# Kernel tuning notes

Measured on AMD Instinct MI355X. Metric: run time of the kernel, lower is better.

## Reference

```python
import jax, jax.numpy as jnp
import numpy as np
import math

N, E, F, H = 8000, 64000, 64, 10
C = F  # out_channels == in_channels in Drug's RAGCN
INV_SQRT_F = 1.0 / math.sqrt(F)


def _glorot(key, shape):
    lim = math.sqrt(6.0 / (shape[0] + shape[1]))
    return jax.random.uniform(key, shape, jnp.float32, -lim, lim)


def setup_inputs() -> dict:
    key = jax.random.key(0)
    ks = jax.random.split(key, 16)
    x = jax.random.normal(ks[0], (N, F), jnp.float32)
    edge_attr = jax.random.normal(ks[1], (E, F), jnp.float32)
    # directed edges with no self loops (module removes them before adding its own)
    src = jax.random.randint(ks[2], (E,), 0, N)
    off = jax.random.randint(ks[3], (E,), 1, N)
    dst = (src + off) % N
    edge_index = jnp.stack([src, dst]).astype(jnp.int32)
    return {
        'x': x,
        'edge_index': edge_index,
        'edge_attr': edge_attr,
        'W_src': _glorot(ks[4], (F, H * C)),
        'Wnq': _glorot(ks[5], (F, F)),
        'Wnk': _glorot(ks[6], (F, F)),
        'Wnv': _glorot(ks[7], (F, F)),
        'Weq': _glorot(ks[8], (F, F)),
        'Wev': _glorot(ks[9], (F, F)),
        'Wek': _glorot(ks[10], (F, F)),
        'W4': _glorot(ks[11], (2 * F, F)),
        'W5': _glorot(ks[12], (F, F)),
        'g1': jnp.ones((F,), jnp.float32),
        'b1': jnp.zeros((F,), jnp.float32),
        'g2': jnp.ones((F,), jnp.float32),
        'b2': jnp.zeros((F,), jnp.float32),
        'bias': jnp.zeros((H * C,), jnp.float32),
    }


def _layernorm(v, g, b):  # torch LayerNorm, eps=0, affine, biased variance
    mu = jnp.mean(v, axis=-1, keepdims=True)
    var = jnp.mean((v - mu) ** 2, axis=-1, keepdims=True)
    return (v - mu) * jax.lax.rsqrt(var) * g + b


def reference(x, edge_index, edge_attr, W_src, Wnq, Wnk, Wnv, Weq, Wev, Wek,
              W4, W5, g1, b1, g2, b2, bias):
    src, dst = edge_index[0], edge_index[1]
    # add_self_loops with fill_value='mean': loop attr = mean of incoming edge_attr
    deg = jax.ops.segment_sum(jnp.ones((E,), x.dtype), dst, num_segments=N)
    loop_attr = jax.ops.segment_sum(edge_attr, dst, num_segments=N) / jnp.maximum(deg, 1.0)[:, None]
    loops = jnp.arange(N, dtype=src.dtype)
    s = jnp.concatenate([src, loops])                  # [Et] edge source index
    ea = jnp.concatenate([edge_attr, loop_attr], 0)    # [Et, F]

    x_src = (x @ W_src).reshape(N, H, C)               # [N, H, C]
    x_j = x_src[s]                                     # gather: [Et, H, C]

    node_K = x_j @ Wnk
    node_V = x_j @ Wnv
    node_Q = x_src @ Wnq
    edge_K = ea @ Weq   # naming follows source: w_e_q feeds edge_K etc.
    edge_V = ea @ Wev
    edge_Q = ea @ Wek

    K_s = jax.ops.segment_sum(node_K + edge_K[:, None, :], s, num_segments=N)
    V_s = jax.ops.segment_sum(node_V + edge_V[:, None, :], s, num_segments=N)
    Q_s = jax.ops.segment_sum(edge_Q, s, num_segments=N)[:, None, :] + node_Q

    qk = jnp.einsum('nhc,nhc->nh', Q_s, K_s) * INV_SQRT_F
    alphi = jax.nn.softmax(qk, axis=1)[:, :, None] * V_s   # softmax over heads dim
    node_update = x_src * alphi                            # [N, H, C]

    # edge update branch
    xj2 = node_update[s]                                   # [Et, H, C]
    edge_rep = jnp.broadcast_to(ea[:, None, :], (s.shape[0], H, F))
    m = jax.nn.relu(jnp.concatenate([edge_rep, xj2], axis=2) @ W4)
    u = _layernorm(m @ W5 + ea[:, None, :], g1, b1)
    eu = _layernorm(u @ W5 + ea[:, None, :], g2, b2)       # source reuses w5

    node_out = node_update.reshape(N, H * C) + bias        # concat heads + bias
    edge_out = eu[:E].mean(axis=1)  # remove appended self loops, mean over heads
    return node_out, edge_out
```

## Files before the change

### kernel.cpp

```cpp
#include <hip/hip_runtime.h>
#include <cstdint>
#include <cstddef>

#define NN 8000
#define EE 64000
#define HH 10

#define OFF_W5T 0
#define OFF_WNQ 4096
#define OFF_WNQL 8192
#define OFF_WNK 12288
#define OFF_WNKL 16384
#define OFF_WNV 20480
#define OFF_WNVL 24576
#define OFF_W4B 28672
#define OFF_W4T 32768
#define OFF_WSRC 36864
#define OFF_WSRCL 77824

typedef __attribute__((ext_vector_type(8))) short bf16x8;
typedef __attribute__((ext_vector_type(4))) float f32x4;
typedef __attribute__((ext_vector_type(4))) unsigned int u32x4;

__device__ __forceinline__ int rfl(int v) { return __builtin_amdgcn_readfirstlane(v); }

__device__ __forceinline__ int cbperm(int k) {
  return 32 * (k >> 5) + 16 * ((k >> 2) & 1) + 4 * ((k >> 3) & 3) + (k & 3);
}

__device__ __forceinline__ unsigned int rne16(float w) {
  unsigned int b = __float_as_uint(w);
  return (b + 0x7FFFu + ((b >> 16) & 1u)) >> 16;
}

__device__ __forceinline__ bf16x8 pack8(f32x4 a, f32x4 b) {
  u32x4 u;
  u[0] = (__float_as_uint(a[1]) & 0xFFFF0000u) | (__float_as_uint(a[0]) >> 16);
  u[1] = (__float_as_uint(a[3]) & 0xFFFF0000u) | (__float_as_uint(a[2]) >> 16);
  u[2] = (__float_as_uint(b[1]) & 0xFFFF0000u) | (__float_as_uint(b[0]) >> 16);
  u[3] = (__float_as_uint(b[3]) & 0xFFFF0000u) | (__float_as_uint(b[2]) >> 16);
  return __builtin_bit_cast(bf16x8, u);
}

__device__ __forceinline__ void split8(f32x4 a, f32x4 b, bf16x8& hi, bf16x8& lo) {
  unsigned int h[4], l[4];
#pragma unroll
  for (int j = 0; j < 2; ++j) {
    unsigned int b0 = __float_as_uint(a[2 * j]);
    unsigned int b1 = __float_as_uint(a[2 * j + 1]);
    h[j] = (b1 & 0xFFFF0000u) | (b0 >> 16);
    float r0 = a[2 * j] - __uint_as_float(b0 & 0xFFFF0000u);
    float r1 = a[2 * j + 1] - __uint_as_float(b1 & 0xFFFF0000u);
    l[j] = (__float_as_uint(r1) & 0xFFFF0000u) | (__float_as_uint(r0) >> 16);
  }
#pragma unroll
  for (int j = 0; j < 2; ++j) {
    unsigned int b0 = __float_as_uint(b[2 * j]);
    unsigned int b1 = __float_as_uint(b[2 * j + 1]);
    h[2 + j] = (b1 & 0xFFFF0000u) | (b0 >> 16);
    float r0 = b[2 * j] - __uint_as_float(b0 & 0xFFFF0000u);
    float r1 = b[2 * j + 1] - __uint_as_float(b1 & 0xFFFF0000u);
    l[2 + j] = (__float_as_uint(r1) & 0xFFFF0000u) | (__float_as_uint(r0) >> 16);
  }
  u32x4 uh = {h[0], h[1], h[2], h[3]};
  u32x4 ul = {l[0], l[1], l[2], l[3]};
  hi = __builtin_bit_cast(bf16x8, uh);
  lo = __builtin_bit_cast(bf16x8, ul);
}

__device__ __forceinline__ f32x4 relu4(f32x4 a, f32x4 b) {
  f32x4 o;
#pragma unroll
  for (int j = 0; j < 4; ++j) o[j] = fmaxf(a[j] + b[j], 0.f);
  return o;
}

__global__ void k_init(float* __restrict__ ws) {
  int t = blockIdx.x * 256 + threadIdx.x;
  int stride = gridDim.x * 256;
  for (int i = t; i < 130 * NN; i += stride)
    ws[i] = (i >= NN && i < 2 * NN) ? 1.0f : 0.0f;
}

__global__ void k_scatter(const int* __restrict__ ei, const float* __restrict__ ea,
                          float* __restrict__ deg, float* __restrict__ dout,
                          float* __restrict__ sum_in, float* __restrict__ sum_src) {
  int t = blockIdx.x * 256 + threadIdx.x;
  if (t >= EE * 64) return;
  int e = t >> 6, f = t & 63;
  int s = ei[e];
  int d = ei[EE + e];
  float v = ea[t];
  atomicAdd(&sum_in[d * 64 + f], v);
  atomicAdd(&sum_src[s * 64 + f], v);
  if (f == 0) {
    atomicAdd(&deg[d], 1.0f);
    atomicAdd(&dout[s], 1.0f);
  }
}

__global__ void k_prepall(const float* __restrict__ Wnq, const float* __restrict__ Wnk,
                          const float* __restrict__ Wnv, const float* __restrict__ W4,
                          const float* __restrict__ Wsrc, const float* __restrict__ W5,
                          const float* __restrict__ g1, const float* __restrict__ b1,
                          float* __restrict__ Cg, float* __restrict__ Cb,
                          unsigned short* __restrict__ wbuf) {
  const int c = blockIdx.x, f = threadIdx.x, y = blockIdx.y;
  if (y == 15) {
    const int cb = cbperm(f);
    float w = W5[cb * 64 + c];
    wbuf[OFF_W5T + c * 64 + f] = (unsigned short)rne16(w);
    float cg = g1[cb] * w;
    float cbb = b1[cb] * w;
#pragma unroll
    for (int off = 1; off < 64; off <<= 1) {
      cg += __shfl_xor(cg, off, 64);
      cbb += __shfl_xor(cbb, off, 64);
    }
    if (f == 0) {
      Cg[c] = cg;
      Cb[c] = cbb;
    }
    return;
  }
  float w;
  int hioff, looff = -1;
  const int cf = c * 64 + f;
  if (y == 0) { w = Wnq[f * 64 + c]; hioff = OFF_WNQ + cf; looff = OFF_WNQL + cf; }
  else if (y == 1) { w = Wnk[f * 64 + c]; hioff = OFF_WNK + cf; looff = OFF_WNKL + cf; }
  else if (y == 2) { w = Wnv[f * 64 + c]; hioff = OFF_WNV + cf; looff = OFF_WNVL + cf; }
  else if (y == 3) { w = W4[(64 + cbperm(f)) * 64 + c]; hioff = OFF_W4B + cf; }
  else if (y == 4) { w = W4[f * 64 + c]; hioff = OFF_W4T + cf; }
  else {
    int h = y - 5;
    w = Wsrc[f * 640 + h * 64 + c];
    hioff = OFF_WSRC + (h * 64 + c) * 64 + f;
    looff = OFF_WSRCL + (h * 64 + c) * 64 + f;
  }
  unsigned int hi = rne16(w);
  wbuf[hioff] = (unsigned short)hi;
  if (looff >= 0) {
    float rest = w - __uint_as_float(hi << 16);
    wbuf[looff] = (unsigned short)rne16(rest);
  }
}

__global__ __launch_bounds__(256) void k_xsrcm(const float* __restrict__ x,
                                               const unsigned short* __restrict__ wbuf,
                                               float* __restrict__ xsrc) {
  const int lane = threadIdx.x & 63;
  const int wv = rfl((int)threadIdx.x >> 6);
  const int g = lane >> 4, r = lane & 15;
  const int h = blockIdx.y;
  const int n = (blockIdx.x * 4 + wv) * 16 + r;
  bf16x8 whi[4][2], wlo[4][2];
#pragma unroll
  for (int mt = 0; mt < 4; ++mt)
#pragma unroll
    for (int ks = 0; ks < 2; ++ks) {
      const int off = (h * 64 + 16 * mt + r) * 64 + 32 * ks + 8 * g;
      whi[mt][ks] = *reinterpret_cast<const bf16x8*>(wbuf + OFF_WSRC + off);
      wlo[mt][ks] = *reinterpret_cast<const bf16x8*>(wbuf + OFF_WSRCL + off);
    }
  const float* xr = x + (size_t)n * 64 + 8 * g;
  bf16x8 xh0, xl0, xh1, xl1;
  split8(*reinterpret_cast<const f32x4*>(xr), *reinterpret_cast<const f32x4*>(xr + 4), xh0, xl0);
  split8(*reinterpret_cast<const f32x4*>(xr + 32), *reinterpret_cast<const f32x4*>(xr + 36), xh1, xl1);
  const size_t base = ((size_t)n * 10 + h) * 64;
#pragma unroll
  for (int mt = 0; mt < 4; ++mt) {
    f32x4 d = {0, 0, 0, 0};
    d = __builtin_amdgcn_mfma_f32_16x16x32_bf16(whi[mt][0], xh0, d, 0, 0, 0);
    d = __builtin_amdgcn_mfma_f32_16x16x32_bf16(whi[mt][1], xh1, d, 0, 0, 0);
    d = __builtin_amdgcn_mfma_f32_16x16x32_bf16(whi[mt][0], xl0, d, 0, 0, 0);
    d = __builtin_amdgcn_mfma_f32_16x16x32_bf16(whi[mt][1], xl1, d, 0, 0, 0);
    d = __builtin_amdgcn_mfma_f32_16x16x32_bf16(wlo[mt][0], xh0, d, 0, 0, 0);
    d = __builtin_amdgcn_mfma_f32_16x16x32_bf16(wlo[mt][1], xh1, d, 0, 0, 0);
    *reinterpret_cast<f32x4*>(xsrc + base + 16 * mt + 4 * g) = d;
  }
}

__global__ __launch_bounds__(256) void k_eaqkv(const float* __restrict__ deg,
                                               const float* __restrict__ sum_in,
                                               const float* __restrict__ sum_src,
                                               const float* __restrict__ Wek,
                                               const float* __restrict__ Weq,
                                               const float* __restrict__ Wev,
                                               float* __restrict__ eaQ,
                                               float* __restrict__ eaK,
                                               float* __restrict__ eaV) {
  const int lane = threadIdx.x & 63;
  const int wv = rfl(threadIdx.x >> 6);
  float wq[64], wk[64], wvv[64];
#pragma unroll
  for (int f = 0; f < 64; ++f) {
    wq[f] = Wek[f * 64 + lane];
    wk[f] = Weq[f * 64 + lane];
    wvv[f] = Wev[f * 64 + lane];
  }
  const int nw = gridDim.x * 4;
  for (int n = blockIdx.x * 4 + wv; n < NN; n += nw) {
    const float* si = sum_in + (size_t)n * 64;
    const float* ss = sum_src + (size_t)n * 64;
    const float invd = 1.0f / fmaxf(deg[n], 1.0f);
    float q0 = 0, q1 = 0, k0 = 0, k1 = 0, v0 = 0, v1 = 0;
#pragma unroll
    for (int f = 0; f < 64; f += 2) {
      float e0 = fmaf(si[f], invd, ss[f]);
      float e1 = fmaf(si[f + 1], invd, ss[f + 1]);
      q0 = fmaf(e0, wq[f], q0);
      q1 = fmaf(e1, wq[f + 1], q1);
      k0 = fmaf(e0, wk[f], k0);
      k1 = fmaf(e1, wk[f + 1], k1);
      v0 = fmaf(e0, wvv[f], v0);
      v1 = fmaf(e1, wvv[f + 1], v1);
    }
    eaQ[(size_t)n * 64 + lane] = q0 + q1;
    eaK[(size_t)n * 64 + lane] = k0 + k1;
    eaV[(size_t)n * 64 + lane] = v0 + v1;
  }
}

__global__ __launch_bounds__(256) void k_qkm(const float* __restrict__ xsrc,
                                             const unsigned short* __restrict__ wbuf,
                                             const float* __restrict__ eaQ,
                                             const float* __restrict__ eaK,
                                             const float* __restrict__ dout,
                                             float* __restrict__ qk) {
  const int lane = threadIdx.x & 63;
  const int wv = rfl((int)threadIdx.x >> 6);
  const int g = lane >> 4, r = lane & 15;
  const int r0 = (blockIdx.x * 4 + wv) * 16;
  const int grow = r0 + r;
  const int n = grow / 10;
  const float* xp = xsrc + (size_t)grow * 64 + 8 * g;
  bf16x8 xh0, xl0, xh1, xl1;
  split8(*reinterpret_cast<const f32x4*>(xp), *reinterpret_cast<const f32x4*>(xp + 4), xh0, xl0);
  split8(*reinterpret_cast<const f32x4*>(xp + 32), *reinterpret_cast<const f32x4*>(xp + 36), xh1, xl1);
  const float dn = dout[n];
  f32x4 qf[4];
#pragma unroll
  for (int mt = 0; mt < 4; ++mt) {
    const int off = (16 * mt + r) * 64 + 8 * g;
    bf16x8 ah0 = *reinterpret_cast<const bf16x8*>(wbuf + OFF_WNQ + off);
    bf16x8 ah1 = *reinterpret_cast<const bf16x8*>(wbuf + OFF_WNQ + off + 32);
    bf16x8 al0 = *reinterpret_cast<const bf16x8*>(wbuf + OFF_WNQL + off);
    bf16x8 al1 = *reinterpret_cast<const bf16x8*>(wbuf + OFF_WNQL + off + 32);
    f32x4 d = {0, 0, 0, 0};
    d = __builtin_amdgcn_mfma_f32_16x16x32_bf16(ah0, xh0, d, 0, 0, 0);
    d = __builtin_amdgcn_mfma_f32_16x16x32_bf16(ah1, xh1, d, 0, 0, 0);
    d = __builtin_amdgcn_mfma_f32_16x16x32_bf16(ah0, xl0, d, 0, 0, 0);
    d = __builtin_amdgcn_mfma_f32_16x16x32_bf16(ah1, xl1, d, 0, 0, 0);
    d = __builtin_amdgcn_mfma_f32_16x16x32_bf16(al0, xh0, d, 0, 0, 0);
    d = __builtin_amdgcn_mfma_f32_16x16x32_bf16(al1, xh1, d, 0, 0, 0);
    qf[mt] = d;
  }
  float p = 0.f;
#pragma unroll
  for (int mt = 0; mt < 4; ++mt) {
    const int off = (16 * mt + r) * 64 + 8 * g;
    bf16x8 ah0 = *reinterpret_cast<const bf16x8*>(wbuf + OFF_WNK + off);
    bf16x8 ah1 = *reinterpret_cast<const bf16x8*>(wbuf + OFF_WNK + off + 32);
    bf16x8 al0 = *reinterpret_cast<const bf16x8*>(wbuf + OFF_WNKL + off);
    bf16x8 al1 = *reinterpret_cast<const bf16x8*>(wbuf + OFF_WNKL + off + 32);
    f32x4 d = {0, 0, 0, 0};
    d = __builtin_amdgcn_mfma_f32_16x16x32_bf16(ah0, xh0, d, 0, 0, 0);
    d = __builtin_amdgcn_mfma_f32_16x16x32_bf16(ah1, xh1, d, 0, 0, 0);
    d = __builtin_amdgcn_mfma_f32_16x16x32_bf16(ah0, xl0, d, 0, 0, 0);
    d = __builtin_amdgcn_mfma_f32_16x16x32_bf16(ah1, xl1, d, 0, 0, 0);
    d = __builtin_amdgcn_mfma_f32_16x16x32_bf16(al0, xh0, d, 0, 0, 0);
    d = __builtin_amdgcn_mfma_f32_16x16x32_bf16(al1, xh1, d, 0, 0, 0);
    f32x4 eq = *reinterpret_cast<const f32x4*>(eaQ + (size_t)n * 64 + 16 * mt + 4 * g);
    f32x4 ek = *reinterpret_cast<const f32x4*>(eaK + (size_t)n * 64 + 16 * mt + 4 * g);
#pragma unroll
    for (int q = 0; q < 4; ++q) p = fmaf(qf[mt][q] + eq[q], fmaf(dn, d[q], ek[q]), p);
  }
  p += __shfl_xor(p, 16, 64);
  p += __shfl_xor(p, 32, 64);
  if (lane < 16) qk[r0 + lane] = p * 0.125f;
}

__global__ void k_softmax(const float* __restrict__ qk, float* __restrict__ sm) {
  int n = blockIdx.x * 256 + threadIdx.x;
  if (n >= NN) return;
  float v[HH];
  float mx = -1e30f;
#pragma unroll
  for (int h = 0; h < HH; ++h) {
    v[h] = qk[n * HH + h];
    mx = fmaxf(mx, v[h]);
  }
  float s = 0;
#pragma unroll
  for (int h = 0; h < HH; ++h) {
    v[h] = expf(v[h] - mx);
    s += v[h];
  }
  float inv = 1.0f / s;
#pragma unroll
  for (int h = 0; h < HH; ++h) sm[n * HH + h] = v[h] * inv;
}

__global__ __launch_bounds__(256) void k_updm(const float* __restrict__ xsrc,
                                              const unsigned short* __restrict__ wbuf,
                                              const float* __restrict__ eaV,
                                              const float* __restrict__ dout,
                                              const float* __restrict__ sm,
                                              const float* __restrict__ bias,
                                              float* __restrict__ node_out,
                                              float* __restrict__ NB) {
  const int lane = threadIdx.x & 63;
  const int wv = rfl((int)threadIdx.x >> 6);
  const int g = lane >> 4, r = lane & 15;
  const int grow = (blockIdx.x * 4 + wv) * 16 + r;
  const int n = grow / 10;
  const int h = grow - 10 * n;
  const float* xp = xsrc + (size_t)grow * 64;
  bf16x8 xh0, xl0, xh1, xl1;
  split8(*reinterpret_cast<const f32x4*>(xp + 8 * g), *reinterpret_cast<const f32x4*>(xp + 8 * g + 4),
         xh0, xl0);
  split8(*reinterpret_cast<const f32x4*>(xp + 8 * g + 32),
         *reinterpret_cast<const f32x4*>(xp + 8 * g + 36), xh1, xl1);
  const float dn = dout[n];
  const float wgt = sm[grow];
  f32x4 nu[4];
#pragma unroll
  for (int mt = 0; mt < 4; ++mt) {
    const int off = (16 * mt + r) * 64 + 8 * g;
    bf16x8 ah0 = *reinterpret_cast<const bf16x8*>(wbuf + OFF_WNV + off);
    bf16x8 ah1 = *reinterpret_cast<const bf16x8*>(wbuf + OFF_WNV + off + 32);
    bf16x8 al0 = *reinterpret_cast<const bf16x8*>(wbuf + OFF_WNVL + off);
    bf16x8 al1 = *reinterpret_cast<const bf16x8*>(wbuf + OFF_WNVL + off + 32);
    f32x4 vf = {0, 0, 0, 0};
    vf = __builtin_amdgcn_mfma_f32_16x16x32_bf16(ah0, xh0, vf, 0, 0, 0);
    vf = __builtin_amdgcn_mfma_f32_16x16x32_bf16(ah1, xh1, vf, 0, 0, 0);
    vf = __builtin_amdgcn_mfma_f32_16x16x32_bf16(ah0, xl0, vf, 0, 0, 0);
    vf = __builtin_amdgcn_mfma_f32_16x16x32_bf16(ah1, xl1, vf, 0, 0, 0);
    vf = __builtin_amdgcn_mfma_f32_16x16x32_bf16(al0, xh0, vf, 0, 0, 0);
    vf = __builtin_amdgcn_mfma_f32_16x16x32_bf16(al1, xh1, vf, 0, 0, 0);
    f32x4 ev = *reinterpret_cast<const f32x4*>(eaV + (size_t)n * 64 + 16 * mt + 4 * g);
    f32x4 xs = *reinterpret_cast<const f32x4*>(xp + 16 * mt + 4 * g);
    f32x4 nn;
#pragma unroll
    for (int q = 0; q < 4; ++q) nn[q] = xs[q] * wgt * fmaf(dn, vf[q], ev[q]);
    nu[mt] = nn;
    f32x4 bs = *reinterpret_cast<const f32x4*>(bias + h * 64 + 16 * mt + 4 * g);
    *reinterpret_cast<f32x4*>(node_out + (size_t)grow * 64 + 16 * mt + 4 * g) = nn + bs;
  }
  bf16x8 nb0 = pack8(nu[0], nu[1]);
  bf16x8 nb1 = pack8(nu[2], nu[3]);
#pragma unroll
  for (int mt = 0; mt < 4; ++mt) {
    const int off = (16 * mt + r) * 64 + 8 * g;
    bf16x8 ba0 = *reinterpret_cast<const bf16x8*>(wbuf + OFF_W4B + off);
    bf16x8 ba1 = *reinterpret_cast<const bf16x8*>(wbuf + OFF_W4B + off + 32);
    f32x4 nf = {0, 0, 0, 0};
    nf = __builtin_amdgcn_mfma_f32_16x16x32_bf16(ba0, nb0, nf, 0, 0, 0);
    nf = __builtin_amdgcn_mfma_f32_16x16x32_bf16(ba1, nb1, nf, 0, 0, 0);
    *reinterpret_cast<f32x4*>(NB + (size_t)grow * 64 + 16 * mt + 4 * g) = nf;
  }
}

__global__ __launch_bounds__(256) void k_edge8(
    const int* __restrict__ ei, const float* __restrict__ ea_g,
    const float* __restrict__ NB, const unsigned short* __restrict__ wbuf,
    const float* __restrict__ Cgp, const float* __restrict__ Cbp,
    const float* __restrict__ g1v, const float* __restrict__ g2v,
    const float* __restrict__ bias2, float* __restrict__ edge_out) {
  const int lane = threadIdx.x & 63;
  const int wv = rfl((int)threadIdx.x >> 6);
  const int g = lane >> 4;
  const int r = lane & 15;
  const int e = (blockIdx.x * 4 + wv) * 16 + r;
  const int src = ei[e];

  bf16x8 whi[4][2];
#pragma unroll
  for (int mt = 0; mt < 4; ++mt)
#pragma unroll
    for (int ks = 0; ks < 2; ++ks)
      whi[mt][ks] = *reinterpret_cast<const bf16x8*>(wbuf + OFF_W5T + (16 * mt + r) * 64 +
                                                     32 * ks + 8 * g);

  const float* EAr = ea_g + (size_t)e * 64;
  const float* ear = EAr + 8 * g;

  f32x4 ad[4];
  {
    bf16x8 eb0 = pack8(*reinterpret_cast<const f32x4*>(ear),
                       *reinterpret_cast<const f32x4*>(ear + 4));
    bf16x8 eb1 = pack8(*reinterpret_cast<const f32x4*>(ear + 32),
                       *reinterpret_cast<const f32x4*>(ear + 36));
#pragma unroll
    for (int mt = 0; mt < 4; ++mt) {
      const int off = (16 * mt + r) * 64 + 8 * g;
      bf16x8 w0 = *reinterpret_cast<const bf16x8*>(wbuf + OFF_W4T + off);
      bf16x8 w1 = *reinterpret_cast<const bf16x8*>(wbuf + OFF_W4T + off + 32);
      f32x4 d = {0, 0, 0, 0};
      d = __builtin_amdgcn_mfma_f32_16x16x32_bf16(w0, eb0, d, 0, 0, 0);
      d = __builtin_amdgcn_mfma_f32_16x16x32_bf16(w1, eb1, d, 0, 0, 0);
      ad[mt] = d;
    }
  }

  const float* NBr = NB + (size_t)src * 640;
  f32x4 outacc[4] = {{0, 0, 0, 0}, {0, 0, 0, 0}, {0, 0, 0, 0}, {0, 0, 0, 0}};

  f32x4 c0 = *reinterpret_cast<const f32x4*>(NBr + 4 * g);
  f32x4 c1 = *reinterpret_cast<const f32x4*>(NBr + 16 + 4 * g);
  f32x4 c2 = *reinterpret_cast<const f32x4*>(NBr + 32 + 4 * g);
  f32x4 c3 = *reinterpret_cast<const f32x4*>(NBr + 48 + 4 * g);

#pragma unroll 1
  for (int h = 0; h < HH; ++h) {
    f32x4 p0, p1, p2, p3;
    if (h < HH - 1) {
      const float* nbn = NBr + (h + 1) * 64;
      p0 = *reinterpret_cast<const f32x4*>(nbn + 4 * g);
      p1 = *reinterpret_cast<const f32x4*>(nbn + 16 + 4 * g);
      p2 = *reinterpret_cast<const f32x4*>(nbn + 32 + 4 * g);
      p3 = *reinterpret_cast<const f32x4*>(nbn + 48 + 4 * g);
    } else {
      p0 = p1 = p2 = p3 = (f32x4){0, 0, 0, 0};
    }

    bf16x8 bhi0 = pack8(relu4(ad[0], c0), relu4(ad[1], c1));
    bf16x8 bhi1 = pack8(relu4(ad[2], c2), relu4(ad[3], c3));

    f32x4 acc1[4];
#pragma unroll
    for (int mt = 0; mt < 4; ++mt) {
      f32x4 a = *reinterpret_cast<const f32x4*>(EAr + 16 * mt + 4 * g);
      a = __builtin_amdgcn_mfma_f32_16x16x32_bf16(whi[mt][0], bhi0, a, 0, 0, 0);
      a = __builtin_amdgcn_mfma_f32_16x16x32_bf16(whi[mt][1], bhi1, a, 0, 0, 0);
      acc1[mt] = a;
    }

    float s = 0.f, s2 = 0.f;
#pragma unroll
    for (int mt = 0; mt < 4; ++mt)
#pragma unroll
      for (int q = 0; q < 4; ++q) {
        float v = acc1[mt][q];
        s += v;
        s2 = fmaf(v, v, s2);
      }
    s += __shfl_xor(s, 16, 64);
    s2 += __shfl_xor(s2, 16, 64);
    s += __shfl_xor(s, 32, 64);
    s2 += __shfl_xor(s2, 32, 64);
    const float mu1 = s * 0.015625f;
    const float rs1 = rsqrtf(fmaxf(s2 * 0.015625f - mu1 * mu1, 1e-30f));

#pragma unroll
    for (int mt = 0; mt < 4; ++mt) {
      f32x4 gv = *reinterpret_cast<const f32x4*>(g1v + 16 * mt + 4 * g);
      acc1[mt] = acc1[mt] * gv * rs1;
    }
    bf16x8 b20 = pack8(acc1[0], acc1[1]);
    bf16x8 b21 = pack8(acc1[2], acc1[3]);

    const float m1r1 = mu1 * rs1;
    f32x4 acc2[4];
#pragma unroll
    for (int mt = 0; mt < 4; ++mt) {
      f32x4 eav = *reinterpret_cast<const f32x4*>(EAr + 16 * mt + 4 * g);
      f32x4 cbv = *reinterpret_cast<const f32x4*>(Cbp + 16 * mt + 4 * g);
      f32x4 cgv = *reinterpret_cast<const f32x4*>(Cgp + 16 * mt + 4 * g);
      f32x4 a = eav + cbv - m1r1 * cgv;
      a = __builtin_amdgcn_mfma_f32_16x16x32_bf16(whi[mt][0], b20, a, 0, 0, 0);
      a = __builtin_amdgcn_mfma_f32_16x16x32_bf16(whi[mt][1], b21, a, 0, 0, 0);
      acc2[mt] = a;
    }

    float t = 0.f, t2 = 0.f;
#pragma unroll
    for (int mt = 0; mt < 4; ++mt)
#pragma unroll
      for (int q = 0; q < 4; ++q) {
        float v = acc2[mt][q];
        t += v;
        t2 = fmaf(v, v, t2);
      }
    t += __shfl_xor(t, 16, 64);
    t2 += __shfl_xor(t2, 16, 64);
    t += __shfl_xor(t, 32, 64);
    t2 += __shfl_xor(t2, 32, 64);
    const float mu2 = t * 0.015625f;
    const float rs2 = rsqrtf(fmaxf(t2 * 0.015625f - mu2 * mu2, 1e-30f));
#pragma unroll
    for (int mt = 0; mt < 4; ++mt) {
      f32x4 g2f = *reinterpret_cast<const f32x4*>(g2v + 16 * mt + 4 * g);
      f32x4 b2f = *reinterpret_cast<const f32x4*>(bias2 + 16 * mt + 4 * g);
      outacc[mt] += (acc2[mt] - mu2) * rs2 * g2f + b2f;
    }

    c0 = p0; c1 = p1; c2 = p2; c3 = p3;
  }

#pragma unroll
  for (int mt = 0; mt < 4; ++mt) {
    f32x4 o = outacc[mt] * 0.1f;
    *reinterpret_cast<f32x4*>(edge_out + (size_t)e * 64 + 16 * mt + 4 * g) = o;
  }
}

extern "C" void kernel_launch(void* const* d_in, const int* in_sizes, int n_in,
                              void* d_out, int out_size, void* d_ws, size_t ws_size,
                              hipStream_t stream) {
  const float* x = (const float*)d_in[0];
  const int* ei = (const int*)d_in[1];
  const float* edge_attr = (const float*)d_in[2];
  const float* W_src = (const float*)d_in[3];
  const float* Wnq = (const float*)d_in[4];
  const float* Wnk = (const float*)d_in[5];
  const float* Wnv = (const float*)d_in[6];
  const float* Weq = (const float*)d_in[7];
  const float* Wev = (const float*)d_in[8];
  const float* Wek = (const float*)d_in[9];
  const float* W4 = (const float*)d_in[10];
  const float* W5 = (const float*)d_in[11];
  const float* g1 = (const float*)d_in[12];
  const float* b1 = (const float*)d_in[13];
  const float* g2 = (const float*)d_in[14];
  const float* b2 = (const float*)d_in[15];
  const float* bias = (const float*)d_in[16];
  (void)in_sizes; (void)n_in; (void)out_size; (void)ws_size;

  float* ws = (float*)d_ws;
  float* deg = ws;
  float* dout = ws + NN;
  float* sum_in = ws + 2 * NN;
  float* sum_src = ws + 66 * NN;
  unsigned short* wbuf = (unsigned short*)(ws + 130 * NN);
  float* eaQ = ws + 194 * NN;
  float* eaK = ws + 258 * NN;
  float* eaV = ws + 322 * NN;
  float* xsrc = ws + 386 * NN;
  float* NB = ws + 1026 * NN;
  float* qk = ws + 1666 * NN;
  float* sm = ws + 1676 * NN;
  float* Cg = ws + 1686 * NN + 64 * EE;
  float* Cb = Cg + 64;

  float* node_out = (float*)d_out;
  float* edge_out = (float*)d_out + (size_t)NN * 640;

  k_init<<<1024, 256, 0, stream>>>(ws);
  k_prepall<<<dim3(64, 16), 64, 0, stream>>>(Wnq, Wnk, Wnv, W4, W_src, W5, g1, b1, Cg, Cb,
                                             wbuf);
  k_scatter<<<EE * 64 / 256, 256, 0, stream>>>(ei, edge_attr, deg, dout, sum_in, sum_src);
  k_xsrcm<<<dim3(NN / 64, 10), 256, 0, stream>>>(x, wbuf, xsrc);
  k_eaqkv<<<250, 256, 0, stream>>>(deg, sum_in, sum_src, Wek, Weq, Wev, eaQ, eaK, eaV);
  k_qkm<<<NN * HH / 64, 256, 0, stream>>>(xsrc, wbuf, eaQ, eaK, dout, qk);
  k_softmax<<<(NN + 255) / 256, 256, 0, stream>>>(qk, sm);
  k_updm<<<NN * HH / 64, 256, 0, stream>>>(xsrc, wbuf, eaV, dout, sm, bias, node_out, NB);
  k_edge8<<<EE / 64, 256, 0, stream>>>(ei, edge_attr, NB, wbuf, Cg, Cb, g1, g2, b2,
                                       edge_out);
}
```

Baseline: 176.1 us.

## Fuse Q/K projection and qk dot into x_src projection kernel; hoist edge-loop loads

Merges the old qk kernel into the x_src projection kernel. The freshly computed x_src tile stays in registers, is split into bf16 hi/lo parts and multiplied by Wnq/Wnk weights stored with a permuted layout (new prep rows 16 and 17), so the x_src re-read and one launch are removed. The edge kernel hoists per-edge constant vectors (edge_attr, Cg, Cb, gamma, beta) out of the head loop and adds a launch bound of two blocks per CU. The trade is higher register pressure in both kernels and a qk indexing layout that must match the new per-node/per-head grid.

Result: faster. 172.0 us (-2.3%).

```diff
diff --git a/kernel.cpp b/kernel.cpp
--- a/kernel.cpp
+++ b/kernel.cpp
@@ -17,6 +17,10 @@
 #define OFF_W4T 32768
 #define OFF_WSRC 36864
 #define OFF_WSRCL 77824
+#define OFF_WNQP 118784
+#define OFF_WNQPL 122880
+#define OFF_WNKP 126976
+#define OFF_WNKPL 131072
 
 typedef __attribute__((ext_vector_type(8))) short bf16x8;
 typedef __attribute__((ext_vector_type(4))) float f32x4;
@@ -131,6 +135,8 @@
   else if (y == 2) { w = Wnv[f * 64 + c]; hioff = OFF_WNV + cf; looff = OFF_WNVL + cf; }
   else if (y == 3) { w = W4[(64 + cbperm(f)) * 64 + c]; hioff = OFF_W4B + cf; }
   else if (y == 4) { w = W4[f * 64 + c]; hioff = OFF_W4T + cf; }
+  else if (y == 16) { w = Wnq[cbperm(f) * 64 + c]; hioff = OFF_WNQP + cf; looff = OFF_WNQPL + cf; }
+  else if (y == 17) { w = Wnk[cbperm(f) * 64 + c]; hioff = OFF_WNKP + cf; looff = OFF_WNKPL + cf; }
   else {
     int h = y - 5;
     w = Wsrc[f * 640 + h * 64 + c];
@@ -145,14 +151,19 @@
   }
 }
 
-__global__ __launch_bounds__(256) void k_xsrcm(const float* __restrict__ x,
+__global__ __launch_bounds__(256) void k_xsrcq(const float* __restrict__ x,
                                                const unsigned short* __restrict__ wbuf,
-                                               float* __restrict__ xsrc) {
+                                               const float* __restrict__ eaQ,
+                                               const float* __restrict__ eaK,
+                                               const float* __restrict__ dout,
+                                               float* __restrict__ xsrc,
+                                               float* __restrict__ qk) {
   const int lane = threadIdx.x & 63;
   const int wv = rfl((int)threadIdx.x >> 6);
   const int g = lane >> 4, r = lane & 15;
   const int h = blockIdx.y;
-  const int n = (blockIdx.x * 4 + wv) * 16 + r;
+  const int n0 = (blockIdx.x * 4 + wv) * 16;
+  const int n = n0 + r;
   bf16x8 whi[4][2], wlo[4][2];
 #pragma unroll
   for (int mt = 0; mt < 4; ++mt)
@@ -167,17 +178,63 @@
   split8(*reinterpret_cast<const f32x4*>(xr), *reinterpret_cast<const f32x4*>(xr + 4), xh0, xl0);
   split8(*reinterpret_cast<const f32x4*>(xr + 32), *reinterpret_cast<const f32x4*>(xr + 36), xh1, xl1);
   const size_t base = ((size_t)n * 10 + h) * 64;
-#pragma unroll
-  for (int mt = 0; mt < 4; ++mt) {
-    f32x4 d = {0, 0, 0, 0};
-    d = __builtin_amdgcn_mfma_f32_16x16x32_bf16(whi[mt][0], xh0, d, 0, 0, 0);
-    d = __builtin_amdgcn_mfma_f32_16x16x32_bf16(whi[mt][1], xh1, d, 0, 0, 0);
-    d = __builtin_amdgcn_mfma_f32_16x16x32_bf16(whi[mt][0], xl0, d, 0, 0, 0);
-    d = __builtin_amdgcn_mfma_f32_16x16x32_bf16(whi[mt][1], xl1, d, 0, 0, 0);
-    d = __builtin_amdgcn_mfma_f32_16x16x32_bf16(wlo[mt][0], xh0, d, 0, 0, 0);
-    d = __builtin_amdgcn_mfma_f32_16x16x32_bf16(wlo[mt][1], xh1, d, 0, 0, 0);
-    *reinterpret_cast<f32x4*>(xsrc + base + 16 * mt + 4 * g) = d;
-  }
+  f32x4 d[4];
+#pragma unroll
+  for (int mt = 0; mt < 4; ++mt) {
+    f32x4 a = {0, 0, 0, 0};
+    a = __builtin_amdgcn_mfma_f32_16x16x32_bf16(whi[mt][0], xh0, a, 0, 0, 0);
+    a = __builtin_amdgcn_mfma_f32_16x16x32_bf16(whi[mt][1], xh1, a, 0, 0, 0);
+    a = __builtin_amdgcn_mfma_f32_16x16x32_bf16(whi[mt][0], xl0, a, 0, 0, 0);
+    a = __builtin_amdgcn_mfma_f32_16x16x32_bf16(whi[mt][1], xl1, a, 0, 0, 0);
+    a = __builtin_amdgcn_mfma_f32_16x16x32_bf16(wlo[mt][0], xh0, a, 0, 0, 0);
+    a = __builtin_amdgcn_mfma_f32_16x16x32_bf16(wlo[mt][1], xh1, a, 0, 0, 0);
+    d[mt] = a;
+    *reinterpret_cast<f32x4*>(xsrc + base + 16 * mt + 4 * g) = a;
+  }
+  bf16x8 dh0, dl0, dh1, dl1;
+  split8(d[0], d[1], dh0, dl0);
+  split8(d[2], d[3], dh1, dl1);
+  const float dn = dout[n];
+  f32x4 qf[4];
+#pragma unroll
+  for (int mt = 0; mt < 4; ++mt) {
+    const int off = (16 * mt + r) * 64 + 8 * g;
+    bf16x8 ah0 = *reinterpret_cast<const bf16x8*>(wbuf + OFF_WNQP + off);
+    bf16x8 ah1 = *reinterpret_cast<const bf16x8*>(wbuf + OFF_WNQP + off + 32);
+    bf16x8 al0 = *reinterpret_cast<const bf16x8*>(wbuf + OFF_WNQPL + off);
+    bf16x8 al1 = *reinterpret_cast<const bf16x8*>(wbuf + OFF_WNQPL + off + 32);
+    f32x4 a = {0, 0, 0, 0};
+    a = __builtin_amdgcn_mfma_f32_16x16x32_bf16(ah0, dh0, a, 0, 0, 0);
+    a = __builtin_amdgcn_mfma_f32_16x16x32_bf16(ah1, dh1, a, 0, 0, 0);
+    a = __builtin_amdgcn_mfma_f32_16x16x32_bf16(ah0, dl0, a, 0, 0, 0);
+    a = __builtin_amdgcn_mfma_f32_16x16x32_bf16(ah1, dl1, a, 0, 0, 0);
+    a = __builtin_amdgcn_mfma_f32_16x16x32_bf16(al0, dh0, a, 0, 0, 0);
+    a = __builtin_amdgcn_mfma_f32_16x16x32_bf16(al1, dh1, a, 0, 0, 0);
+    qf[mt] = a;
+  }
+  float p = 0.f;
+#pragma unroll
+  for (int mt = 0; mt < 4; ++mt) {
+    const int off = (16 * mt + r) * 64 + 8 * g;
+    bf16x8 ah0 = *reinterpret_cast<const bf16x8*>(wbuf + OFF_WNKP + off);
+    bf16x8 ah1 = *reinterpret_cast<const bf16x8*>(wbuf + OFF_WNKP + off + 32);
+    bf16x8 al0 = *reinterpret_cast<const bf16x8*>(wbuf + OFF_WNKPL + off);
+    bf16x8 al1 = *reinterpret_cast<const bf16x8*>(wbuf + OFF_WNKPL + off + 32);
+    f32x4 a = {0, 0, 0, 0};
+    a = __builtin_amdgcn_mfma_f32_16x16x32_bf16(ah0, dh0, a, 0, 0, 0);
+    a = __builtin_amdgcn_mfma_f32_16x16x32_bf16(ah1, dh1, a, 0, 0, 0);
+    a = __builtin_amdgcn_mfma_f32_16x16x32_bf16(ah0, dl0, a, 0, 0, 0);
+    a = __builtin_amdgcn_mfma_f32_16x16x32_bf16(ah1, dl1, a, 0, 0, 0);
+    a = __builtin_amdgcn_mfma_f32_16x16x32_bf16(al0, dh0, a, 0, 0, 0);
+    a = __builtin_amdgcn_mfma_f32_16x16x32_bf16(al1, dh1, a, 0, 0, 0);
+    f32x4 eq = *reinterpret_cast<const f32x4*>(eaQ + (size_t)n * 64 + 16 * mt + 4 * g);
+    f32x4 ek = *reinterpret_cast<const f32x4*>(eaK + (size_t)n * 64 + 16 * mt + 4 * g);
+#pragma unroll
+    for (int q = 0; q < 4; ++q) p = fmaf(qf[mt][q] + eq[q], fmaf(dn, a[q], ek[q]), p);
+  }
+  p += __shfl_xor(p, 16, 64);
+  p += __shfl_xor(p, 32, 64);
+  if (lane < 16) qk[(size_t)(n0 + lane) * HH + h] = p * 0.125f;
 }
 
 __global__ __launch_bounds__(256) void k_eaqkv(const float* __restrict__ deg,
@@ -219,65 +276,6 @@
     eaK[(size_t)n * 64 + lane] = k0 + k1;
     eaV[(size_t)n * 64 + lane] = v0 + v1;
   }
-}
-
-__global__ __launch_bounds__(256) void k_qkm(const float* __restrict__ xsrc,
-                                             const unsigned short* __restrict__ wbuf,
-                                             const float* __restrict__ eaQ,
-                                             const float* __restrict__ eaK,
-                                             const float* __restrict__ dout,
-                                             float* __restrict__ qk) {
-  const int lane = threadIdx.x & 63;
-  const int wv = rfl((int)threadIdx.x >> 6);
-  const int g = lane >> 4, r = lane & 15;
-  const int r0 = (blockIdx.x * 4 + wv) * 16;
-  const int grow = r0 + r;
-  const int n = grow / 10;
-  const float* xp = xsrc + (size_t)grow * 64 + 8 * g;
-  bf16x8 xh0, xl0, xh1, xl1;
-  split8(*reinterpret_cast<const f32x4*>(xp), *reinterpret_cast<const f32x4*>(xp + 4), xh0, xl0);
-  split8(*reinterpret_cast<const f32x4*>(xp + 32), *reinterpret_cast<const f32x4*>(xp + 36), xh1, xl1);
-  const float dn = dout[n];
-  f32x4 qf[4];
-#pragma unroll
-  for (int mt = 0; mt < 4; ++mt) {
-    const int off = (16 * mt + r) * 64 + 8 * g;
-    bf16x8 ah0 = *reinterpret_cast<const bf16x8*>(wbuf + OFF_WNQ + off);
-    bf16x8 ah1 = *reinterpret_cast<const bf16x8*>(wbuf + OFF_WNQ + off + 32);
-    bf16x8 al0 = *reinterpret_cast<const bf16x8*>(wbuf + OFF_WNQL + off);
-    bf16x8 al1 = *reinterpret_cast<const bf16x8*>(wbuf + OFF_WNQL + off + 32);
-    f32x4 d = {0, 0, 0, 0};
-    d = __builtin_amdgcn_mfma_f32_16x16x32_bf16(ah0, xh0, d, 0, 0, 0);
-    d = __builtin_amdgcn_mfma_f32_16x16x32_bf16(ah1, xh1, d, 0, 0, 0);
-    d = __builtin_amdgcn_mfma_f32_16x16x32_bf16(ah0, xl0, d, 0, 0, 0);
-    d = __builtin_amdgcn_mfma_f32_16x16x32_bf16(ah1, xl1, d, 0, 0, 0);
-    d = __builtin_amdgcn_mfma_f32_16x16x32_bf16(al0, xh0, d, 0, 0, 0);
-    d = __builtin_amdgcn_mfma_f32_16x16x32_bf16(al1, xh1, d, 0, 0, 0);
-    qf[mt] = d;
-  }
-  float p = 0.f;
-#pragma unroll
-  for (int mt = 0; mt < 4; ++mt) {
-    const int off = (16 * mt + r) * 64 + 8 * g;
-    bf16x8 ah0 = *reinterpret_cast<const bf16x8*>(wbuf + OFF_WNK + off);
-    bf16x8 ah1 = *reinterpret_cast<const bf16x8*>(wbuf + OFF_WNK + off + 32);
-    bf16x8 al0 = *reinterpret_cast<const bf16x8*>(wbuf + OFF_WNKL + off);
-    bf16x8 al1 = *reinterpret_cast<const bf16x8*>(wbuf + OFF_WNKL + off + 32);
-    f32x4 d = {0, 0, 0, 0};
-    d = __builtin_amdgcn_mfma_f32_16x16x32_bf16(ah0, xh0, d, 0, 0, 0);
-    d = __builtin_amdgcn_mfma_f32_16x16x32_bf16(ah1, xh1, d, 0, 0, 0);
-    d = __builtin_amdgcn_mfma_f32_16x16x32_bf16(ah0, xl0, d, 0, 0, 0);
-    d = __builtin_amdgcn_mfma_f32_16x16x32_bf16(ah1, xl1, d, 0, 0, 0);
-    d = __builtin_amdgcn_mfma_f32_16x16x32_bf16(al0, xh0, d, 0, 0, 0);
-    d = __builtin_amdgcn_mfma_f32_16x16x32_bf16(al1, xh1, d, 0, 0, 0);
-    f32x4 eq = *reinterpret_cast<const f32x4*>(eaQ + (size_t)n * 64 + 16 * mt + 4 * g);
-    f32x4 ek = *reinterpret_cast<const f32x4*>(eaK + (size_t)n * 64 + 16 * mt + 4 * g);
-#pragma unroll
-    for (int q = 0; q < 4; ++q) p = fmaf(qf[mt][q] + eq[q], fmaf(dn, d[q], ek[q]), p);
-  }
-  p += __shfl_xor(p, 16, 64);
-  p += __shfl_xor(p, 32, 64);
-  if (lane < 16) qk[r0 + lane] = p * 0.125f;
 }
 
 __global__ void k_softmax(const float* __restrict__ qk, float* __restrict__ sm) {
@@ -361,7 +359,7 @@
   }
 }
 
-__global__ __launch_bounds__(256) void k_edge8(
+__global__ __launch_bounds__(256, 2) void k_edge9(
     const int* __restrict__ ei, const float* __restrict__ ea_g,
     const float* __restrict__ NB, const unsigned short* __restrict__ wbuf,
     const float* __restrict__ Cgp, const float* __restrict__ Cbp,
@@ -385,6 +383,17 @@
   const float* EAr = ea_g + (size_t)e * 64;
   const float* ear = EAr + 8 * g;
 
+  f32x4 eav[4], cbv[4], cgv[4], g1r[4], g2r[4], b2r[4];
+#pragma unroll
+  for (int mt = 0; mt < 4; ++mt) {
+    eav[mt] = *reinterpret_cast<const f32x4*>(EAr + 16 * mt + 4 * g);
+    cbv[mt] = *reinterpret_cast<const f32x4*>(Cbp + 16 * mt + 4 * g);
+    cgv[mt] = *reinterpret_cast<const f32x4*>(Cgp + 16 * mt + 4 * g);
+    g1r[mt] = *reinterpret_cast<const f32x4*>(g1v + 16 * mt + 4 * g);
+    g2r[mt] = *reinterpret_cast<const f32x4*>(g2v + 16 * mt + 4 * g);
+    b2r[mt] = *reinterpret_cast<const f32x4*>(bias2 + 16 * mt + 4 * g);
+  }
+
   f32x4 ad[4];
   {
     bf16x8 eb0 = pack8(*reinterpret_cast<const f32x4*>(ear),
@@ -430,7 +439,7 @@
     f32x4 acc1[4];
 #pragma unroll
     for (int mt = 0; mt < 4; ++mt) {
-      f32x4 a = *reinterpret_cast<const f32x4*>(EAr + 16 * mt + 4 * g);
+      f32x4 a = eav[mt];
       a = __builtin_amdgcn_mfma_f32_16x16x32_bf16(whi[mt][0], bhi0, a, 0, 0, 0);
       a = __builtin_amdgcn_mfma_f32_16x16x32_bf16(whi[mt][1], bhi1, a, 0, 0, 0);
       acc1[mt] = a;
@@ -453,10 +462,7 @@
     const float rs1 = rsqrtf(fmaxf(s2 * 0.015625f - mu1 * mu1, 1e-30f));
 
 #pragma unroll
-    for (int mt = 0; mt < 4; ++mt) {
-      f32x4 gv = *reinterpret_cast<const f32x4*>(g1v + 16 * mt + 4 * g);
-      acc1[mt] = acc1[mt] * gv * rs1;
-    }
+    for (int mt = 0; mt < 4; ++mt) acc1[mt] = acc1[mt] * g1r[mt] * rs1;
     bf16x8 b20 = pack8(acc1[0], acc1[1]);
     bf16x8 b21 = pack8(acc1[2], acc1[3]);
 
@@ -464,10 +470,7 @@
     f32x4 acc2[4];
 #pragma unroll
     for (int mt = 0; mt < 4; ++mt) {
-      f32x4 eav = *reinterpret_cast<const f32x4*>(EAr + 16 * mt + 4 * g);
-      f32x4 cbv = *reinterpret_cast<const f32x4*>(Cbp + 16 * mt + 4 * g);
-      f32x4 cgv = *reinterpret_cast<const f32x4*>(Cgp + 16 * mt + 4 * g);
-      f32x4 a = eav + cbv - m1r1 * cgv;
+      f32x4 a = eav[mt] + cbv[mt] - m1r1 * cgv[mt];
       a = __builtin_amdgcn_mfma_f32_16x16x32_bf16(whi[mt][0], b20, a, 0, 0, 0);
       a = __builtin_amdgcn_mfma_f32_16x16x32_bf16(whi[mt][1], b21, a, 0, 0, 0);
       acc2[mt] = a;
@@ -489,11 +492,8 @@
     const float mu2 = t * 0.015625f;
     const float rs2 = rsqrtf(fmaxf(t2 * 0.015625f - mu2 * mu2, 1e-30f));
 #pragma unroll
-    for (int mt = 0; mt < 4; ++mt) {
-      f32x4 g2f = *reinterpret_cast<const f32x4*>(g2v + 16 * mt + 4 * g);
-      f32x4 b2f = *reinterpret_cast<const f32x4*>(bias2 + 16 * mt + 4 * g);
-      outacc[mt] += (acc2[mt] - mu2) * rs2 * g2f + b2f;
-    }
+    for (int mt = 0; mt < 4; ++mt)
+      outacc[mt] += (acc2[mt] - mu2) * rs2 * g2r[mt] + b2r[mt];
 
     c0 = p0; c1 = p1; c2 = p2; c3 = p3;
   }
@@ -547,14 +547,13 @@
   float* edge_out = (float*)d_out + (size_t)NN * 640;
 
   k_init<<<1024, 256, 0, stream>>>(ws);
-  k_prepall<<<dim3(64, 16), 64, 0, stream>>>(Wnq, Wnk, Wnv, W4, W_src, W5, g1, b1, Cg, Cb,
+  k_prepall<<<dim3(64, 18), 64, 0, stream>>>(Wnq, Wnk, Wnv, W4, W_src, W5, g1, b1, Cg, Cb,
                                              wbuf);
   k_scatter<<<EE * 64 / 256, 256, 0, stream>>>(ei, edge_attr, deg, dout, sum_in, sum_src);
-  k_xsrcm<<<dim3(NN / 64, 10), 256, 0, stream>>>(x, wbuf, xsrc);
   k_eaqkv<<<250, 256, 0, stream>>>(deg, sum_in, sum_src, Wek, Weq, Wev, eaQ, eaK, eaV);
-  k_qkm<<<NN * HH / 64, 256, 0, stream>>>(xsrc, wbuf, eaQ, eaK, dout, qk);
+  k_xsrcq<<<dim3(NN / 64, 10), 256, 0, stream>>>(x, wbuf, eaQ, eaK, dout, xsrc, qk);
   k_softmax<<<(NN + 255) / 256, 256, 0, stream>>>(qk, sm);
   k_updm<<<NN * HH / 64, 256, 0, stream>>>(xsrc, wbuf, eaV, dout, sm, bias, node_out, NB);
-  k_edge8<<<EE / 64, 256, 0, stream>>>(ei, edge_attr, NB, wbuf, Cg, Cb, g1, g2, b2,
+  k_edge9<<<EE / 64, 256, 0, stream>>>(ei, edge_attr, NB, wbuf, Cg, Cb, g1, g2, b2,
                                        edge_out);
 }
```
